# Optimization experiments

Measured on AMD Instinct MI355X. Metric: run time of the kernel, lower is better.

## Reference

```python
import jax, jax.numpy as jnp
import numpy as np

INPUT_CHANNELS = 6
RESERVOIR_SIZE = 256
SPECTRAL_RADIUS = 0.9
SPARSITY = 0.8
BATCH = 256
SEQ_LEN = 512


def _make_reservoir_weights(seed=0):
    rng = np.random.RandomState(seed)
    W_res = rng.randn(RESERVOIR_SIZE, RESERVOIR_SIZE).astype(np.float32)
    mask = (rng.rand(RESERVOIR_SIZE, RESERVOIR_SIZE) > SPARSITY).astype(np.float32)
    W_res = W_res * mask
    cur_radius = np.abs(np.linalg.eigvals(W_res)).max()
    if cur_radius > 0:
        W_res = W_res * (SPECTRAL_RADIUS / cur_radius)
    return W_res.astype(np.float32)


def setup_inputs() -> dict:
    key = jax.random.key(0)
    k_x, k_in = jax.random.split(key)
    x = jax.random.normal(k_x, (BATCH, SEQ_LEN, INPUT_CHANNELS), dtype=jnp.float32)
    W_in = jax.random.normal(k_in, (INPUT_CHANNELS, RESERVOIR_SIZE), dtype=jnp.float32) * 0.1
    W_res = jnp.asarray(_make_reservoir_weights())
    return {"x": x, "W_in": W_in, "W_res": W_res}


def reference(x, W_in, W_res):
    # x: [B, T, C] -> x_proj: [B, T, R]
    x_proj = jnp.einsum("btc,cr->btr", x, W_in)
    B = x.shape[0]
    R = W_res.shape[0]
    h0 = jnp.zeros((B, R), dtype=x.dtype)

    def step(h, xp_t):
        # xp_t: [B, R]
        h_new = jnp.tanh(xp_t + h @ W_res)
        return h_new, h_new

    # scan over time: xs must be time-major [T, B, R]
    _, h_seq = jax.lax.scan(step, h0, jnp.swapaxes(x_proj, 0, 1))
    return jnp.swapaxes(h_seq, 0, 1)  # [B, T, R]
```

## Files before the change

### kernel.cpp

```cpp
#include <hip/hip_runtime.h>

#define BATCH 256
#define SEQ_T 512
#define CIN   6
#define RES   256

__global__ __launch_bounds__(1024, 4)
void esn_scan_kernel(const float* __restrict__ x,
                     const float* __restrict__ W_in,
                     const float* __restrict__ W_res,
                     float* __restrict__ out) {
    __shared__ float h[2][RES];
    __shared__ float part[8][RES];

    const int tid = threadIdx.x;
    const int b   = blockIdx.x;
    const int r   = tid & 127;
    const int kk  = tid >> 7;

    float w0[32], w1[32];
    #pragma unroll
    for (int j = 0; j < 32; ++j) {
        const float2 wv = ((const float2*)W_res)[(32 * kk + j) * 128 + r];
        w0[j] = wv.x;
        w1[j] = wv.y;
    }
    #pragma unroll
    for (int j = 0; j < 32; ++j) {
        asm volatile("" : "+v"(w0[j]), "+v"(w1[j]));
    }

    float win[CIN];
    if (tid < RES) {
        #pragma unroll
        for (int c = 0; c < CIN; ++c) win[c] = W_in[c * RES + tid];
    }

    if (tid < RES) h[0][tid] = 0.0f;
    __syncthreads();

    const float* xb = x + (size_t)b * SEQ_T * CIN;
    float*       ob = out + (size_t)b * SEQ_T * RES;

    int p = 0;
    for (int t = 0; t < SEQ_T; ++t) {
        float hv = h[p][32 * kk + (tid & 31)];
        float a0 = 0.0f, a1 = 0.0f;
        #pragma unroll
        for (int j = 0; j < 32; ++j) {
            const float hj = __int_as_float(
                __builtin_amdgcn_readlane(__float_as_int(hv), j));
            a0 = fmaf(hj, w0[j], a0);
            a1 = fmaf(hj, w1[j], a1);
        }
        ((float2*)&part[kk][0])[r] = make_float2(a0, a1);

        float xv[CIN];
        if (tid < RES) {
            #pragma unroll
            for (int c = 0; c < CIN; ++c) xv[c] = xb[t * CIN + c];
        }
        __syncthreads();

        if (tid < RES) {
            float s = 0.0f;
            #pragma unroll
            for (int c = 0; c < CIN; ++c) s = fmaf(xv[c], win[c], s);
            #pragma unroll
            for (int q = 0; q < 8; ++q) s += part[q][tid];
            float e  = __expf(2.0f * s);
            float hn = 1.0f - 2.0f * __builtin_amdgcn_rcpf(e + 1.0f);
            h[1 - p][tid]     = hn;
            ob[t * RES + tid] = hn;
        }
        __syncthreads();
        p ^= 1;
    }
}

extern "C" void kernel_launch(void* const* d_in, const int* in_sizes, int n_in,
                              void* d_out, int out_size, void* d_ws, size_t ws_size,
                              hipStream_t stream) {
    const float* x     = (const float*)d_in[0];
    const float* W_in  = (const float*)d_in[1];
    const float* W_res = (const float*)d_in[2];
    float*       out   = (float*)d_out;

    esn_scan_kernel<<<BATCH, 1024, 0, stream>>>(x, W_in, W_res, out);
}
```

Measured before the change: 485.1 us.

## Halve block size with four outputs per thread and inline-asm scalar FMACs

Each block now uses 512 threads (8 waves), and each thread holds 32 float4 weight values and computes four output columns instead of two. The inner product uses inline v_fmac with the broadcast h value in an SGPR. The x loads are hoisted ahead of the matvec so all threads issue them. The aim is to cut the number of waves synchronising at each timestep barrier and raise FMA work per readlane, at the cost of more VGPRs per thread and less latency hiding.

```diff
diff --git a/kernel.cpp b/kernel.cpp
--- a/kernel.cpp
+++ b/kernel.cpp
@@ -5,7 +5,10 @@
 #define CIN   6
 #define RES   256
 
-__global__ __launch_bounds__(1024, 4)
+#define FMAC_SV(acc, s_h, v_w) \
+    asm("v_fmac_f32 %0, %1, %2" : "+v"(acc) : "s"(s_h), "v"(v_w))
+
+__global__ __launch_bounds__(512, 2)
 void esn_scan_kernel(const float* __restrict__ x,
                      const float* __restrict__ W_in,
                      const float* __restrict__ W_res,
@@ -13,22 +16,16 @@
     __shared__ float h[2][RES];
     __shared__ float part[8][RES];
 
-    const int tid = threadIdx.x;
-    const int b   = blockIdx.x;
-    const int r   = tid & 127;
-    const int kk  = tid >> 7;
+    const int tid  = threadIdx.x;
+    const int b    = blockIdx.x;
+    const int w    = tid >> 6;
+    const int g    = tid & 63;
+    const int lane = tid & 31;
 
-    float w0[32], w1[32];
+    float4 wv[32];
     #pragma unroll
-    for (int j = 0; j < 32; ++j) {
-        const float2 wv = ((const float2*)W_res)[(32 * kk + j) * 128 + r];
-        w0[j] = wv.x;
-        w1[j] = wv.y;
-    }
-    #pragma unroll
-    for (int j = 0; j < 32; ++j) {
-        asm volatile("" : "+v"(w0[j]), "+v"(w1[j]));
-    }
+    for (int j = 0; j < 32; ++j)
+        wv[j] = ((const float4*)W_res)[(32 * w + j) * 64 + g];
 
     float win[CIN];
     if (tid < RES) {
@@ -44,22 +41,22 @@
 
     int p = 0;
     for (int t = 0; t < SEQ_T; ++t) {
-        float hv = h[p][32 * kk + (tid & 31)];
-        float a0 = 0.0f, a1 = 0.0f;
+        float xv[CIN];
+        #pragma unroll
+        for (int c = 0; c < CIN; ++c) xv[c] = xb[t * CIN + c];
+
+        float hv = h[p][32 * w + lane];
+        float a0 = 0.0f, a1 = 0.0f, a2 = 0.0f, a3 = 0.0f;
         #pragma unroll
         for (int j = 0; j < 32; ++j) {
             const float hj = __int_as_float(
                 __builtin_amdgcn_readlane(__float_as_int(hv), j));
-            a0 = fmaf(hj, w0[j], a0);
-            a1 = fmaf(hj, w1[j], a1);
+            FMAC_SV(a0, hj, wv[j].x);
+            FMAC_SV(a1, hj, wv[j].y);
+            FMAC_SV(a2, hj, wv[j].z);
+            FMAC_SV(a3, hj, wv[j].w);
         }
-        ((float2*)&part[kk][0])[r] = make_float2(a0, a1);
-
-        float xv[CIN];
-        if (tid < RES) {
-            #pragma unroll
-            for (int c = 0; c < CIN; ++c) xv[c] = xb[t * CIN + c];
-        }
+        ((float4*)&part[w][0])[g] = make_float4(a0, a1, a2, a3);
         __syncthreads();
 
         if (tid < RES) {
@@ -86,5 +83,5 @@
     const float* W_res = (const float*)d_in[2];
     float*       out   = (float*)d_out;
 
-    esn_scan_kernel<<<BATCH, 1024, 0, stream>>>(x, W_in, W_res, out);
+    esn_scan_kernel<<<BATCH, 512, 0, stream>>>(x, W_in, W_res, out);
 }
```

New measurement: 606.5 us. +25.0%, slower.
